# Performance work log

Hardware: AMD Instinct MI355X
Metric: run time of the kernel (lower is better)

Reference implementation:

```python
import jax, jax.numpy as jnp
import numpy as np

B, T_IN, T_OUT = 512, 256, 128
V, N, EH, DH, SD = 256, 1024, 64, 128, 32


def _lstm_scan(gx_seq, W_hh, h0, c0):
    """gx_seq: (T, B, 4H) precomputed input-side gates (incl. bias).
    PyTorch LSTMCell gate order: i, f, g, o."""
    def step(carry, gx):
        h, c = carry
        g = gx + h @ W_hh.T                       # (B, 4H)
        i, f, gg, o = jnp.split(g, 4, axis=-1)
        c2 = jax.nn.sigmoid(f) * c + jax.nn.sigmoid(i) * jnp.tanh(gg)
        h2 = jax.nn.sigmoid(o) * jnp.tanh(c2)
        return (h2, c2), h2
    (hT, cT), hs = jax.lax.scan(step, (h0, c0), gx_seq)
    return hT, hs


def _forward(inp_onehot, zia, tgt, fortza,
             enc_Wih, enc_Whh, enc_b, sg_W, sg_b,
             Wc_W, Wc_b, dec_Wih, dec_Whh, dec_b, out_W, out_b):
    Bb = inp_onehot.shape[0]
    dt = inp_onehot.dtype
    # ---- encoder: input projection hoisted out of the recurrence ----
    # enc_in = concat([x_t, zia]); zia is constant over t, so its gate
    # contribution is computed once (same math as the per-step cat+GEMM).
    Wx, Wz = enc_Wih[:, :V], enc_Wih[:, V:]          # (4EH,V), (4EH,N)
    gx_const = zia @ Wz.T + enc_b                    # (B, 4EH)
    gx_enc = jnp.einsum('btv,gv->tbg', inp_onehot, Wx) + gx_const[None]
    h0 = jnp.zeros((Bb, EH), dt)
    h_enc, _ = _lstm_scan(gx_enc, enc_Whh, h0, h0)   # (B, EH)
    # ---- soul update ----
    sg = jnp.concatenate([h_enc, fortza], axis=-1) @ sg_W.T + sg_b
    gate = jax.nn.sigmoid(sg[:, :SD])
    update = jnp.tanh(sg[:, SD:])
    fortza_new = gate * fortza + (1.0 - gate) * update
    # ---- decoder init ----
    dh0 = jnp.tanh(jnp.concatenate([h_enc, zia], axis=-1) @ Wc_W.T + Wc_b)
    dc0 = jnp.zeros_like(dh0)
    # ---- decoder recurrence ----
    gx_dec = jnp.einsum('btv,gv->tbg', tgt, dec_Wih) + dec_b
    _, dhs = _lstm_scan(gx_dec, dec_Whh, dh0, dc0)   # (T_out, B, DH)
    # ---- output projection: split cat([dh, fortza_new]) @ W.T ----
    Wd, Wf = out_W[:, :DH], out_W[:, DH:]
    logits = (jnp.einsum('tbh,vh->btv', dhs, Wd)
              + (fortza_new @ Wf.T)[:, None, :] + out_b)
    return logits, fortza_new


def setup_inputs() -> dict:
    key = jax.random.key(0)
    ks = jax.random.split(key, 20)
    f32 = jnp.float32
    def nrm(k, shape, s=0.05):
        return jax.random.normal(k, shape, f32) * s
    inp_idx = jax.random.randint(ks[0], (B, T_IN), 0, V)
    tgt_idx = jax.random.randint(ks[1], (B, T_OUT), 0, V)
    return {
        'inp_onehot': jax.nn.one_hot(inp_idx, V, dtype=f32),
        'zia': jax.random.uniform(ks[2], (B, N), f32),
        'tgt': jax.nn.one_hot(tgt_idx, V, dtype=f32),
        'fortza': nrm(ks[3], (B, SD), 0.5),
        'enc_Wih': nrm(ks[4], (4 * EH, V + N)),
        'enc_Whh': nrm(ks[5], (4 * EH, EH)),
        'enc_b': nrm(ks[6], (4 * EH,)),
        'sg_W': nrm(ks[7], (2 * SD, EH + SD)),
        'sg_b': nrm(ks[8], (2 * SD,)),
        'Wc_W': nrm(ks[9], (DH, EH + N)),
        'Wc_b': nrm(ks[10], (DH,)),
        'dec_Wih': nrm(ks[11], (4 * DH, V)),
        'dec_Whh': nrm(ks[12], (4 * DH, DH)),
        'dec_b': nrm(ks[13], (4 * DH,)),
        'out_W': nrm(ks[14], (V, DH + SD)),
        'out_b': nrm(ks[15], (V,)),
    }


def reference(inp_onehot, zia, tgt, fortza,
              enc_Wih, enc_Whh, enc_b, sg_W, sg_b,
              Wc_W, Wc_b, dec_Wih, dec_Whh, dec_b, out_W, out_b):
    return _forward(inp_onehot, zia, tgt, fortza,
                    enc_Wih, enc_Whh, enc_b, sg_W, sg_b,
                    Wc_W, Wc_b, dec_Wih, dec_Whh, dec_b, out_W, out_b)
```

## Files before the change

### kernel.cpp

```cpp
#include <hip/hip_runtime.h>
#include <hip/hip_bf16.h>

#define BATCH 512
#define TIN   256
#define TOUT  128
#define VOC   256
#define NZ    1024
#define EHID  64
#define DHID  128
#define SDIM  32

typedef __attribute__((ext_vector_type(8))) short bf16x8;
typedef __attribute__((ext_vector_type(4))) float f32x4;

__device__ __forceinline__ float bf2f(unsigned short u) {
  return __uint_as_float(((unsigned)u) << 16);
}
__device__ __forceinline__ unsigned short f2bf(float f) {
  unsigned u = __float_as_uint(f);
  u = u + 0x7FFFu + ((u >> 16) & 1u);
  return (unsigned short)(u >> 16);
}
__device__ __forceinline__ float sigf(float x) { return 1.0f / (1.0f + __expf(-x)); }
__device__ __forceinline__ float tanh_(float x) { return 1.0f - 2.0f / (1.0f + __expf(2.0f * x)); }

__device__ __forceinline__ bf16x8 pack8(float4 a, float4 b) {
  bf16x8 r;
  r[0] = (short)f2bf(a.x); r[1] = (short)f2bf(a.y);
  r[2] = (short)f2bf(a.z); r[3] = (short)f2bf(a.w);
  r[4] = (short)f2bf(b.x); r[5] = (short)f2bf(b.y);
  r[6] = (short)f2bf(b.z); r[7] = (short)f2bf(b.w);
  return r;
}

__device__ __forceinline__ void dev_findidx(const float* __restrict__ src,
                                            int pos, int lane,
                                            int* __restrict__ out) {
  float4 v = ((const float4*)src)[(size_t)pos * 64 + lane];
  int comp = v.x > 0.5f ? 0 : (v.y > 0.5f ? 1 : (v.z > 0.5f ? 2 : 3));
  bool hit = (v.x > 0.5f) || (v.y > 0.5f) || (v.z > 0.5f) || (v.w > 0.5f);
  int cand = hit ? lane * 4 + comp : (1 << 30);
#pragma unroll
  for (int off = 32; off > 0; off >>= 1) {
    int o = __shfl_xor(cand, off);
    cand = cand < o ? cand : o;
  }
  if (lane == 0) out[pos] = cand < VOC ? cand : VOC - 1;
}

__global__ __launch_bounds__(256) void k_pre(
    const float* __restrict__ enc_Wih, const float* __restrict__ enc_b,
    const float* __restrict__ inp_onehot, const float* __restrict__ zia,
    float* __restrict__ WxT, float* __restrict__ gxc, int* __restrict__ enc_idx) {
  int blk = blockIdx.x, tid = threadIdx.x;
  if (blk < 64) {
    __shared__ float T[32][36];
    int r = tid >> 3, c = (tid & 7) * 4;
    int g0 = (blk >> 3) * 32, v0 = (blk & 7) * 32;
    float4 v = *(const float4*)(enc_Wih + (size_t)(g0 + r) * (VOC + NZ) + v0 + c);
    float bias = enc_b[g0 + r];
    T[c + 0][r] = v.x + bias; T[c + 1][r] = v.y + bias;
    T[c + 2][r] = v.z + bias; T[c + 3][r] = v.w + bias;
    __syncthreads();
    *(float4*)(WxT + (size_t)(v0 + r) * 256 + g0 + c) = *(const float4*)&T[r][c];
  } else if (blk < 192) {
    __shared__ float As[32][36], Bs[32][36];
    int q = blk - 64;
    int b0 = (q & 15) * 32, g0 = (q >> 4) * 32;
    int ldr = tid >> 3, ldc = (tid & 7) * 4;
    int tx = tid & 15, ty = tid >> 4;
    float a00 = 0.f, a01 = 0.f, a10 = 0.f, a11 = 0.f;
    for (int kc = 0; kc < NZ; kc += 32) {
      float4 av = *(const float4*)(zia + (size_t)(b0 + ldr) * NZ + kc + ldc);
      float4 bv = *(const float4*)(enc_Wih + (size_t)(g0 + ldr) * (VOC + NZ) + VOC + kc + ldc);
      __syncthreads();
      As[ldc + 0][ldr] = av.x; As[ldc + 1][ldr] = av.y;
      As[ldc + 2][ldr] = av.z; As[ldc + 3][ldr] = av.w;
      Bs[ldc + 0][ldr] = bv.x; Bs[ldc + 1][ldr] = bv.y;
      Bs[ldc + 2][ldr] = bv.z; Bs[ldc + 3][ldr] = bv.w;
      __syncthreads();
#pragma unroll
      for (int k = 0; k < 32; ++k) {
        float x0 = As[k][tx * 2], x1 = As[k][tx * 2 + 1];
        float y0 = Bs[k][ty * 2], y1 = Bs[k][ty * 2 + 1];
        a00 += x0 * y0; a01 += x0 * y1; a10 += x1 * y0; a11 += x1 * y1;
      }
    }
    float* o = gxc + (size_t)(b0 + tx * 2) * 256 + g0 + ty * 2;
    o[0] = a00; o[1] = a01; o[256] = a10; o[257] = a11;
  } else {
    int pos = (blk - 192) * 4 + (tid >> 6);
    if (pos < BATCH * TIN) dev_findidx(inp_onehot, pos, tid & 63, enc_idx);
  }
}

#define ESTR 72
__global__ __launch_bounds__(256) void k_enc_fused(
    const float* __restrict__ enc_Whh, const float* __restrict__ WxT,
    const float* __restrict__ gxc, const int* __restrict__ enc_idx,
    float* __restrict__ h_enc,
    const float* __restrict__ dec_Wih, const float* __restrict__ dec_b,
    const float* __restrict__ out_W, const float* __restrict__ tgt,
    float* __restrict__ WdecT, float* __restrict__ WdT, int* __restrict__ dec_idx) {
  int blk = blockIdx.x, tid = threadIdx.x;
  if (blk < 128) {
    __shared__ unsigned short hA[2][16 * ESTR];
    __shared__ int idx_s[4][TIN];
    int b0 = blk * 4;
    int w = tid >> 6, lane = tid & 63, n = lane & 15, quad = lane >> 4;
    int j = w * 16 + n;

    bf16x8 Bf[4][2];
#pragma unroll
    for (int ty = 0; ty < 4; ++ty)
#pragma unroll
      for (int kb = 0; kb < 2; ++kb) {
        const float* s = enc_Whh + (size_t)(ty * 64 + j) * EHID + kb * 32 + quad * 8;
        Bf[ty][kb] = pack8(*(const float4*)s, *(const float4*)(s + 4));
      }
    for (int i = tid; i < 16 * ESTR; i += 256) { hA[0][i] = 0; hA[1][i] = 0; }
    for (int i = tid; i < 4 * TIN; i += 256)
      idx_s[i >> 8][i & 255] = enc_idx[(size_t)(b0 + (i >> 8)) * TIN + (i & 255)];
    float gc[4];
#pragma unroll
    for (int ty = 0; ty < 4; ++ty) gc[ty] = gxc[(size_t)(b0 + quad) * 256 + ty * 64 + j];
    __syncthreads();

    float gx[4];
    {
      int id0 = idx_s[quad][0];
#pragma unroll
      for (int ty = 0; ty < 4; ++ty) gx[ty] = WxT[(size_t)id0 * 256 + ty * 64 + j];
    }
    float c0 = 0.0f, h = 0.0f;
    for (int t = 0; t < TIN; ++t) {
      const unsigned short* cur = hA[t & 1];
      bf16x8 a[2];
#pragma unroll
      for (int kb = 0; kb < 2; ++kb)
        a[kb] = *(const bf16x8*)(cur + n * ESTR + kb * 32 + quad * 8);
      float gxn[4];
      int tn = (t + 1 < TIN) ? t + 1 : t;
      int idn = idx_s[quad][tn];
#pragma unroll
      for (int ty = 0; ty < 4; ++ty) gxn[ty] = WxT[(size_t)idn * 256 + ty * 64 + j];
      f32x4 acc[4];
#pragma unroll
      for (int ty = 0; ty < 4; ++ty) {
        f32x4 z; z[0] = gx[ty] + gc[ty]; z[1] = 0.f; z[2] = 0.f; z[3] = 0.f;
        z = __builtin_amdgcn_mfma_f32_16x16x32_bf16(a[0], Bf[ty][0], z, 0, 0, 0);
        z = __builtin_amdgcn_mfma_f32_16x16x32_bf16(a[1], Bf[ty][1], z, 0, 0, 0);
        acc[ty] = z;
      }
      float gi = acc[0][0], gf = acc[1][0], gg = acc[2][0], go = acc[3][0];
      c0 = sigf(gf) * c0 + sigf(gi) * tanh_(gg);
      h = sigf(go) * tanh_(c0);
      hA[(t + 1) & 1][(quad * 4) * ESTR + j] = f2bf(h);
      gx[0] = gxn[0]; gx[1] = gxn[1]; gx[2] = gxn[2]; gx[3] = gxn[3];
      __syncthreads();
    }
    h_enc[(size_t)(b0 + quad) * EHID + j] = h;
  } else if (blk < 256) {
    __shared__ float T[32][36];
    int q = blk - 128;
    int r = tid >> 3, c = (tid & 7) * 4;
    int g0 = (q >> 3) * 32, v0 = (q & 7) * 32;
    float4 v = *(const float4*)(dec_Wih + (size_t)(g0 + r) * VOC + v0 + c);
    float bias = dec_b[g0 + r];
    T[c + 0][r] = v.x + bias; T[c + 1][r] = v.y + bias;
    T[c + 2][r] = v.z + bias; T[c + 3][r] = v.w + bias;
    __syncthreads();
    *(float4*)(WdecT + (size_t)(v0 + r) * 512 + g0 + c) = *(const float4*)&T[r][c];
  } else if (blk < 288) {
    __shared__ float T2[32][36];
    int q = blk - 256;
    int r = tid >> 3, c = (tid & 7) * 4;
    int v0 = (q >> 2) * 32, k0 = (q & 3) * 32;
    float4 v = *(const float4*)(out_W + (size_t)(v0 + r) * (DHID + SDIM) + k0 + c);
    T2[c + 0][r] = v.x; T2[c + 1][r] = v.y; T2[c + 2][r] = v.z; T2[c + 3][r] = v.w;
    __syncthreads();
    *(float4*)(WdT + (size_t)(k0 + r) * 256 + v0 + c) = *(const float4*)&T2[r][c];
  } else {
    int pos = (blk - 288) * 4 + (tid >> 6);
    if (pos < BATCH * TOUT) dev_findidx(tgt, pos, tid & 63, dec_idx);
  }
}

__global__ __launch_bounds__(256) void k_mid(
    const float* __restrict__ h_enc, const float* __restrict__ fortza,
    const float* __restrict__ sg_W, const float* __restrict__ sg_b,
    const float* __restrict__ out_W, const float* __restrict__ out_b,
    const float* __restrict__ zia, const float* __restrict__ Wc_W,
    const float* __restrict__ Wc_b,
    float* __restrict__ out_fortza, float* __restrict__ fout,
    float* __restrict__ dh0) {
  int blk = blockIdx.x, tid = threadIdx.x;
  if (blk < 512) {
    __shared__ float hf[EHID], fz[SDIM], sg_s[2 * SDIM], fn[SDIM];
    int b = blk;
    if (tid < EHID) hf[tid] = h_enc[b * EHID + tid];
    if (tid >= EHID && tid < EHID + SDIM)
      fz[tid - EHID] = fortza[(size_t)b * SDIM + (tid - EHID)];
    __syncthreads();
    if (tid < 2 * SDIM) {
      float acc = sg_b[tid];
      const float* row = sg_W + (size_t)tid * (EHID + SDIM);
      for (int k = 0; k < EHID; ++k) acc += hf[k] * row[k];
      for (int jj = 0; jj < SDIM; ++jj) acc += fz[jj] * row[EHID + jj];
      sg_s[tid] = acc;
    }
    __syncthreads();
    if (tid < SDIM) {
      float gate = sigf(sg_s[tid]);
      float upd = tanh_(sg_s[SDIM + tid]);
      float v = gate * fz[tid] + (1.0f - gate) * upd;
      fn[tid] = v;
      out_fortza[(size_t)b * SDIM + tid] = v;
    }
    __syncthreads();
    {
      float acc = out_b[tid];
      const float* row = out_W + (size_t)tid * (DHID + SDIM) + DHID;
      for (int jj = 0; jj < SDIM; ++jj) acc += fn[jj] * row[jj];
      fout[b * VOC + tid] = acc;
    }
  } else {
    __shared__ float As[32][36], Bs[32][36];
    int q = blk - 512;
    int b0 = (q & 15) * 32, v0 = (q >> 4) * 32;
    int ldr = tid >> 3, ldc = (tid & 7) * 4;
    int tx = tid & 15, ty = tid >> 4;
    float a00 = 0.f, a01 = 0.f, a10 = 0.f, a11 = 0.f;
    for (int kc = 0; kc < EHID + NZ; kc += 32) {
      float4 av;
      if (kc < EHID)
        av = *(const float4*)(h_enc + (size_t)(b0 + ldr) * EHID + kc + ldc);
      else
        av = *(const float4*)(zia + (size_t)(b0 + ldr) * NZ + (kc - EHID) + ldc);
      float4 bv = *(const float4*)(Wc_W + (size_t)(v0 + ldr) * (EHID + NZ) + kc + ldc);
      __syncthreads();
      As[ldc + 0][ldr] = av.x; As[ldc + 1][ldr] = av.y;
      As[ldc + 2][ldr] = av.z; As[ldc + 3][ldr] = av.w;
      Bs[ldc + 0][ldr] = bv.x; Bs[ldc + 1][ldr] = bv.y;
      Bs[ldc + 2][ldr] = bv.z; Bs[ldc + 3][ldr] = bv.w;
      __syncthreads();
#pragma unroll
      for (int k = 0; k < 32; ++k) {
        float x0 = As[k][tx * 2], x1 = As[k][tx * 2 + 1];
        float y0 = Bs[k][ty * 2], y1 = Bs[k][ty * 2 + 1];
        a00 += x0 * y0; a01 += x0 * y1; a10 += x1 * y0; a11 += x1 * y1;
      }
    }
    float bb0 = Wc_b[v0 + ty * 2], bb1 = Wc_b[v0 + ty * 2 + 1];
    float* o = dh0 + (size_t)(b0 + tx * 2) * DHID + v0 + ty * 2;
    o[0] = tanh_(a00 + bb0); o[1] = tanh_(a01 + bb1);
    o[DHID] = tanh_(a10 + bb0); o[DHID + 1] = tanh_(a11 + bb1);
  }
}

#define DSTR 136
__global__ __launch_bounds__(512) void k_dec_scan(
    const float* __restrict__ dec_Whh, const float* __restrict__ WdecT,
    const int* __restrict__ dec_idx, const float* __restrict__ dh0,
    unsigned short* __restrict__ dhs) {
  __shared__ unsigned short hA[2][16 * DSTR];
  __shared__ int idx_s[4][TOUT];
  int b0 = blockIdx.x * 4;
  int tid = threadIdx.x;
  int w = tid >> 6, lane = tid & 63, n = lane & 15, quad = lane >> 4;
  int j0 = w * 16, j = j0 + n;

  bf16x8 Bf[4][4];
#pragma unroll
  for (int ty = 0; ty < 4; ++ty)
#pragma unroll
    for (int kb = 0; kb < 4; ++kb) {
      const float* src = dec_Whh + (size_t)(ty * 128 + j0 + n) * DHID + kb * 32 + quad * 8;
      Bf[ty][kb] = pack8(*(const float4*)src, *(const float4*)(src + 4));
    }
  for (int i = tid; i < 16 * DSTR; i += 512) {
    int m = i / DSTR, k = i - m * DSTR;
    float v = (k < DHID && (m & 3) == 0) ? dh0[(size_t)(b0 + (m >> 2)) * DHID + k] : 0.0f;
    hA[0][i] = f2bf(v);
    hA[1][i] = 0;
  }
  for (int i = tid; i < 4 * TOUT; i += 512)
    idx_s[i >> 7][i & 127] = dec_idx[(size_t)(b0 + (i >> 7)) * TOUT + (i & 127)];
  __syncthreads();

  float gx[4];
  {
    int id0 = idx_s[quad][0];
#pragma unroll
    for (int ty = 0; ty < 4; ++ty) gx[ty] = WdecT[(size_t)id0 * 512 + ty * 128 + j];
  }
  float c0 = 0.0f;
  for (int t = 0; t < TOUT; ++t) {
    const unsigned short* cur = hA[t & 1];
    bf16x8 a[4];
#pragma unroll
    for (int kb = 0; kb < 4; ++kb)
      a[kb] = *(const bf16x8*)(cur + n * DSTR + kb * 32 + quad * 8);
    float gxn[4];
    int tn = (t + 1 < TOUT) ? t + 1 : t;
    int idn = idx_s[quad][tn];
#pragma unroll
    for (int ty = 0; ty < 4; ++ty) gxn[ty] = WdecT[(size_t)idn * 512 + ty * 128 + j];
    f32x4 acc[4];
#pragma unroll
    for (int ty = 0; ty < 4; ++ty) {
      f32x4 z; z[0] = gx[ty]; z[1] = 0.f; z[2] = 0.f; z[3] = 0.f;
#pragma unroll
      for (int kb = 0; kb < 4; ++kb)
        z = __builtin_amdgcn_mfma_f32_16x16x32_bf16(a[kb], Bf[ty][kb], z, 0, 0, 0);
      acc[ty] = z;
    }
    float gi = acc[0][0], gf = acc[1][0], gg = acc[2][0], go = acc[3][0];
    c0 = sigf(gf) * c0 + sigf(gi) * tanh_(gg);
    float h = sigf(go) * tanh_(c0);
    unsigned short hb = f2bf(h);
    hA[(t + 1) & 1][(quad * 4) * DSTR + j] = hb;
    dhs[((size_t)t * BATCH + b0 + quad) * DHID + j] = hb;
    gx[0] = gxn[0]; gx[1] = gxn[1]; gx[2] = gxn[2]; gx[3] = gxn[3];
    __syncthreads();
  }
}

__global__ __launch_bounds__(256) void k_logits(const unsigned short* __restrict__ dhs,
                                                const float* __restrict__ WdT,
                                                const float* __restrict__ fout,
                                                float* __restrict__ out) {
  __shared__ float s[DHID * 64];
  int r0 = blockIdx.x * 64;
  int t = r0 / BATCH;
  int b0 = r0 % BATCH;
  int tid = threadIdx.x;
  for (int i = tid; i < 64 * DHID; i += 256) {
    int m = i >> 7;
    int k = i & 127;
    s[k * 64 + m] = bf2f(dhs[(size_t)(r0 + m) * DHID + k]);
  }
  __syncthreads();
  int v4 = tid & 63;
  int mg = tid >> 6;
  float4 acc[16];
#pragma unroll
  for (int m = 0; m < 16; ++m) acc[m] = make_float4(0.f, 0.f, 0.f, 0.f);
  for (int k = 0; k < DHID; ++k) {
    float4 wv = ((const float4*)(WdT + k * 256))[v4];
    const float4* sk = (const float4*)(s + k * 64 + mg * 16);
#pragma unroll
    for (int jj = 0; jj < 4; ++jj) {
      float4 h4 = sk[jj];
      acc[jj * 4 + 0].x += h4.x * wv.x; acc[jj * 4 + 0].y += h4.x * wv.y;
      acc[jj * 4 + 0].z += h4.x * wv.z; acc[jj * 4 + 0].w += h4.x * wv.w;
      acc[jj * 4 + 1].x += h4.y * wv.x; acc[jj * 4 + 1].y += h4.y * wv.y;
      acc[jj * 4 + 1].z += h4.y * wv.z; acc[jj * 4 + 1].w += h4.y * wv.w;
      acc[jj * 4 + 2].x += h4.z * wv.x; acc[jj * 4 + 2].y += h4.z * wv.y;
      acc[jj * 4 + 2].z += h4.z * wv.z; acc[jj * 4 + 2].w += h4.z * wv.w;
      acc[jj * 4 + 3].x += h4.w * wv.x; acc[jj * 4 + 3].y += h4.w * wv.y;
      acc[jj * 4 + 3].z += h4.w * wv.z; acc[jj * 4 + 3].w += h4.w * wv.w;
    }
  }
#pragma unroll
  for (int m = 0; m < 16; ++m) {
    int bb = b0 + mg * 16 + m;
    float4 fo = ((const float4*)(fout + bb * VOC))[v4];
    float4 r;
    r.x = acc[m].x + fo.x;
    r.y = acc[m].y + fo.y;
    r.z = acc[m].z + fo.z;
    r.w = acc[m].w + fo.w;
    ((float4*)(out + ((size_t)bb * TOUT + t) * VOC))[v4] = r;
  }
}

extern "C" void kernel_launch(void* const* d_in, const int* in_sizes, int n_in,
                              void* d_out, int out_size, void* d_ws, size_t ws_size,
                              hipStream_t stream) {
  const float* inp_onehot = (const float*)d_in[0];
  const float* zia     = (const float*)d_in[1];
  const float* tgt     = (const float*)d_in[2];
  const float* fortza  = (const float*)d_in[3];
  const float* enc_Wih = (const float*)d_in[4];
  const float* enc_Whh = (const float*)d_in[5];
  const float* enc_b   = (const float*)d_in[6];
  const float* sg_W    = (const float*)d_in[7];
  const float* sg_b    = (const float*)d_in[8];
  const float* Wc_W    = (const float*)d_in[9];
  const float* Wc_b    = (const float*)d_in[10];
  const float* dec_Wih = (const float*)d_in[11];
  const float* dec_Whh = (const float*)d_in[12];
  const float* dec_b   = (const float*)d_in[13];
  const float* out_W   = (const float*)d_in[14];
  const float* out_b   = (const float*)d_in[15];
  float* out = (float*)d_out;

  float* ws = (float*)d_ws;
  int* enc_idx  = (int*)d_ws;
  int* dec_idx  = enc_idx + BATCH * TIN;
  float* WxT    = ws + 196608;
  float* WdecT  = ws + 262144;
  float* WdT    = ws + 393216;
  float* gxc    = ws + 425984;
  float* h_enc  = ws + 557056;
  float* dh0    = ws + 589824;
  float* fout   = ws + 655360;
  unsigned short* dhs = (unsigned short*)(ws + 786432);

  k_pre<<<192 + BATCH * TIN / 4, 256, 0, stream>>>(
      enc_Wih, enc_b, inp_onehot, zia, WxT, gxc, enc_idx);
  k_enc_fused<<<288 + BATCH * TOUT / 4, 256, 0, stream>>>(
      enc_Whh, WxT, gxc, enc_idx, h_enc,
      dec_Wih, dec_b, out_W, tgt, WdecT, WdT, dec_idx);
  k_mid<<<576, 256, 0, stream>>>(h_enc, fortza, sg_W, sg_b, out_W, out_b,
                                 zia, Wc_W, Wc_b,
                                 out + (size_t)BATCH * TOUT * VOC, fout, dh0);
  k_dec_scan<<<BATCH / 4, 512, 0, stream>>>(dec_Whh, WdecT, dec_idx, dh0, dhs);
  k_logits<<<TOUT * BATCH / 64, 256, 0, stream>>>(dhs, WdT, fout, out);
}
```

Before: 568.6 us.

## Fuse output logits projection into decoder scan and batch one-hot index search

The output projection is folded into the decoder recurrence. Each step runs MFMA on the previous hidden state held in LDS against bf16 out_W fragments kept in registers and writes the logits directly, so the bf16 dhs buffer and the separate logits kernel go away. The one-hot index search blocks now process 16 positions per wavefront, which cuts the block count. The trade-off is extra MFMA work and scattered global stores on the serial recurrence path, more register pressure, and the logits GEMM now running in bf16 on only 128 blocks.

```diff
diff --git a/kernel.cpp b/kernel.cpp
--- a/kernel.cpp
+++ b/kernel.cpp
@@ -89,8 +89,11 @@
     float* o = gxc + (size_t)(b0 + tx * 2) * 256 + g0 + ty * 2;
     o[0] = a00; o[1] = a01; o[256] = a10; o[257] = a11;
   } else {
-    int pos = (blk - 192) * 4 + (tid >> 6);
-    if (pos < BATCH * TIN) dev_findidx(inp_onehot, pos, tid & 63, enc_idx);
+    int widx = (blk - 192) * 4 + (tid >> 6);
+    int lane = tid & 63;
+#pragma unroll 2
+    for (int i = 0; i < 16; ++i)
+      dev_findidx(inp_onehot, widx * 16 + i, lane, enc_idx);
   }
 }
 
@@ -181,8 +184,11 @@
     __syncthreads();
     *(float4*)(WdT + (size_t)(k0 + r) * 256 + v0 + c) = *(const float4*)&T2[r][c];
   } else {
-    int pos = (blk - 288) * 4 + (tid >> 6);
-    if (pos < BATCH * TOUT) dev_findidx(tgt, pos, tid & 63, dec_idx);
+    int widx = (blk - 288) * 4 + (tid >> 6);
+    int lane = tid & 63;
+#pragma unroll 2
+    for (int i = 0; i < 16; ++i)
+      dev_findidx(tgt, widx * 16 + i, lane, dec_idx);
   }
 }
 
@@ -259,10 +265,11 @@
 }
 
 #define DSTR 136
-__global__ __launch_bounds__(512) void k_dec_scan(
+__global__ __launch_bounds__(512) void k_dec_logits(
     const float* __restrict__ dec_Whh, const float* __restrict__ WdecT,
     const int* __restrict__ dec_idx, const float* __restrict__ dh0,
-    unsigned short* __restrict__ dhs) {
+    const float* __restrict__ WdT, const float* __restrict__ fout,
+    float* __restrict__ out) {
   __shared__ unsigned short hA[2][16 * DSTR];
   __shared__ int idx_s[4][TOUT];
   int b0 = blockIdx.x * 4;
@@ -278,6 +285,21 @@
       const float* src = dec_Whh + (size_t)(ty * 128 + j0 + n) * DHID + kb * 32 + quad * 8;
       Bf[ty][kb] = pack8(*(const float4*)src, *(const float4*)(src + 4));
     }
+  bf16x8 BfL[2][4];
+  float fo[2];
+#pragma unroll
+  for (int p = 0; p < 2; ++p) {
+    int v = (w * 2 + p) * 16 + n;
+#pragma unroll
+    for (int kb = 0; kb < 4; ++kb) {
+      const float* src = WdT + (size_t)(kb * 32 + quad * 8) * 256 + v;
+      bf16x8 r;
+#pragma unroll
+      for (int i = 0; i < 8; ++i) r[i] = (short)f2bf(src[i * 256]);
+      BfL[p][kb] = r;
+    }
+    fo[p] = fout[(size_t)(b0 + quad) * VOC + v];
+  }
   for (int i = tid; i < 16 * DSTR; i += 512) {
     int m = i / DSTR, k = i - m * DSTR;
     float v = (k < DHID && (m & 3) == 0) ? dh0[(size_t)(b0 + (m >> 2)) * DHID + k] : 0.0f;
@@ -301,6 +323,16 @@
 #pragma unroll
     for (int kb = 0; kb < 4; ++kb)
       a[kb] = *(const bf16x8*)(cur + n * DSTR + kb * 32 + quad * 8);
+    if (t > 0) {
+#pragma unroll
+      for (int p = 0; p < 2; ++p) {
+        f32x4 z; z[0] = fo[p]; z[1] = 0.f; z[2] = 0.f; z[3] = 0.f;
+#pragma unroll
+        for (int kb = 0; kb < 4; ++kb)
+          z = __builtin_amdgcn_mfma_f32_16x16x32_bf16(a[kb], BfL[p][kb], z, 0, 0, 0);
+        out[((size_t)(b0 + quad) * TOUT + (t - 1)) * VOC + (w * 2 + p) * 16 + n] = z[0];
+      }
+    }
     float gxn[4];
     int tn = (t + 1 < TOUT) ? t + 1 : t;
     int idn = idx_s[quad][tn];
@@ -318,60 +350,24 @@
     float gi = acc[0][0], gf = acc[1][0], gg = acc[2][0], go = acc[3][0];
     c0 = sigf(gf) * c0 + sigf(gi) * tanh_(gg);
     float h = sigf(go) * tanh_(c0);
-    unsigned short hb = f2bf(h);
-    hA[(t + 1) & 1][(quad * 4) * DSTR + j] = hb;
-    dhs[((size_t)t * BATCH + b0 + quad) * DHID + j] = hb;
+    hA[(t + 1) & 1][(quad * 4) * DSTR + j] = f2bf(h);
     gx[0] = gxn[0]; gx[1] = gxn[1]; gx[2] = gxn[2]; gx[3] = gxn[3];
     __syncthreads();
   }
-}
-
-__global__ __launch_bounds__(256) void k_logits(const unsigned short* __restrict__ dhs,
-                                                const float* __restrict__ WdT,
-                                                const float* __restrict__ fout,
-                                                float* __restrict__ out) {
-  __shared__ float s[DHID * 64];
-  int r0 = blockIdx.x * 64;
-  int t = r0 / BATCH;
-  int b0 = r0 % BATCH;
-  int tid = threadIdx.x;
-  for (int i = tid; i < 64 * DHID; i += 256) {
-    int m = i >> 7;
-    int k = i & 127;
-    s[k * 64 + m] = bf2f(dhs[(size_t)(r0 + m) * DHID + k]);
-  }
-  __syncthreads();
-  int v4 = tid & 63;
-  int mg = tid >> 6;
-  float4 acc[16];
-#pragma unroll
-  for (int m = 0; m < 16; ++m) acc[m] = make_float4(0.f, 0.f, 0.f, 0.f);
-  for (int k = 0; k < DHID; ++k) {
-    float4 wv = ((const float4*)(WdT + k * 256))[v4];
-    const float4* sk = (const float4*)(s + k * 64 + mg * 16);
-#pragma unroll
-    for (int jj = 0; jj < 4; ++jj) {
-      float4 h4 = sk[jj];
-      acc[jj * 4 + 0].x += h4.x * wv.x; acc[jj * 4 + 0].y += h4.x * wv.y;
-      acc[jj * 4 + 0].z += h4.x * wv.z; acc[jj * 4 + 0].w += h4.x * wv.w;
-      acc[jj * 4 + 1].x += h4.y * wv.x; acc[jj * 4 + 1].y += h4.y * wv.y;
-      acc[jj * 4 + 1].z += h4.y * wv.z; acc[jj * 4 + 1].w += h4.y * wv.w;
-      acc[jj * 4 + 2].x += h4.z * wv.x; acc[jj * 4 + 2].y += h4.z * wv.y;
-      acc[jj * 4 + 2].z += h4.z * wv.z; acc[jj * 4 + 2].w += h4.z * wv.w;
-      acc[jj * 4 + 3].x += h4.w * wv.x; acc[jj * 4 + 3].y += h4.w * wv.y;
-      acc[jj * 4 + 3].z += h4.w * wv.z; acc[jj * 4 + 3].w += h4.w * wv.w;
-    }
-  }
-#pragma unroll
-  for (int m = 0; m < 16; ++m) {
-    int bb = b0 + mg * 16 + m;
-    float4 fo = ((const float4*)(fout + bb * VOC))[v4];
-    float4 r;
-    r.x = acc[m].x + fo.x;
-    r.y = acc[m].y + fo.y;
-    r.z = acc[m].z + fo.z;
-    r.w = acc[m].w + fo.w;
-    ((float4*)(out + ((size_t)bb * TOUT + t) * VOC))[v4] = r;
+  {
+    const unsigned short* cur = hA[0];
+    bf16x8 a[4];
+#pragma unroll
+    for (int kb = 0; kb < 4; ++kb)
+      a[kb] = *(const bf16x8*)(cur + n * DSTR + kb * 32 + quad * 8);
+#pragma unroll
+    for (int p = 0; p < 2; ++p) {
+      f32x4 z; z[0] = fo[p]; z[1] = 0.f; z[2] = 0.f; z[3] = 0.f;
+#pragma unroll
+      for (int kb = 0; kb < 4; ++kb)
+        z = __builtin_amdgcn_mfma_f32_16x16x32_bf16(a[kb], BfL[p][kb], z, 0, 0, 0);
+      out[((size_t)(b0 + quad) * TOUT + (TOUT - 1)) * VOC + (w * 2 + p) * 16 + n] = z[0];
+    }
   }
 }
 
@@ -406,16 +402,15 @@
   float* h_enc  = ws + 557056;
   float* dh0    = ws + 589824;
   float* fout   = ws + 655360;
-  unsigned short* dhs = (unsigned short*)(ws + 786432);
-
-  k_pre<<<192 + BATCH * TIN / 4, 256, 0, stream>>>(
+
+  k_pre<<<192 + 2048, 256, 0, stream>>>(
       enc_Wih, enc_b, inp_onehot, zia, WxT, gxc, enc_idx);
-  k_enc_fused<<<288 + BATCH * TOUT / 4, 256, 0, stream>>>(
+  k_enc_fused<<<288 + 1024, 256, 0, stream>>>(
       enc_Whh, WxT, gxc, enc_idx, h_enc,
       dec_Wih, dec_b, out_W, tgt, WdecT, WdT, dec_idx);
   k_mid<<<576, 256, 0, stream>>>(h_enc, fortza, sg_W, sg_b, out_W, out_b,
                                  zia, Wc_W, Wc_b,
                                  out + (size_t)BATCH * TOUT * VOC, fout, dh0);
-  k_dec_scan<<<BATCH / 4, 512, 0, stream>>>(dec_Whh, WdecT, dec_idx, dh0, dhs);
-  k_logits<<<TOUT * BATCH / 64, 256, 0, stream>>>(dhs, WdT, fout, out);
-}
+  k_dec_logits<<<BATCH / 4, 512, 0, stream>>>(dec_Whh, WdecT, dec_idx, dh0,
+                                              WdT, fout, out);
+}
```

Result: faster. 539.5 us (-5.1%).
